# Optimization experiments

Measured on AMD Instinct MI355X. Metric: run time of the kernel, lower is better.

The kernel has to match this reference:

```python
import jax, jax.numpy as jnp
import numpy as np

N_NODES = 100000
N_EDGES = 1600000
IN_FEATS = 128
N_HIDDEN = 32
N_CLASSES = 47
HEADS = (4, 4)
NEG_SLOPE = 0.2


def setup_inputs() -> dict:
    key = jax.random.key(0)
    ks = jax.random.split(key, 12)
    x = jax.random.normal(ks[0], (N_NODES, IN_FEATS), dtype=jnp.float32)
    src = jax.random.randint(ks[1], (N_EDGES,), 0, N_NODES)
    dst = jax.random.randint(ks[2], (N_EDGES,), 0, N_NODES)
    inverse_idx = jax.random.randint(ks[3], (N_NODES,), 0, N_NODES)
    h1 = HEADS[0] * N_HIDDEN
    s1 = 1.0 / np.sqrt(IN_FEATS)
    W1 = jax.random.normal(ks[4], (IN_FEATS, h1), dtype=jnp.float32) * s1
    al1 = jax.random.normal(ks[5], (HEADS[0], N_HIDDEN), dtype=jnp.float32) * 0.1
    ar1 = jax.random.normal(ks[6], (HEADS[0], N_HIDDEN), dtype=jnp.float32) * 0.1
    b1 = jnp.zeros((h1,), dtype=jnp.float32)
    h2 = HEADS[1] * N_CLASSES
    s2 = 1.0 / np.sqrt(h1)
    W2 = jax.random.normal(ks[7], (h1, h2), dtype=jnp.float32) * s2
    al2 = jax.random.normal(ks[8], (HEADS[1], N_CLASSES), dtype=jnp.float32) * 0.1
    ar2 = jax.random.normal(ks[9], (HEADS[1], N_CLASSES), dtype=jnp.float32) * 0.1
    b2 = jnp.zeros((h2,), dtype=jnp.float32)
    return {"x": x, "src": src, "dst": dst, "inverse_idx": inverse_idx,
            "W1": W1, "al1": al1, "ar1": ar1, "b1": b1,
            "W2": W2, "al2": al2, "ar2": ar2, "b2": b2}


def gat_conv(h, src, dst, W, al, ar, b, heads, out_dim, apply_elu):
    # DGL GATConv (feat_drop=attn_drop=0, eval mode):
    # projected per-head features, edge attention, per-dst softmax, aggregate.
    feat = (h @ W).reshape(-1, heads, out_dim)               # (N, H, D)
    el = jnp.einsum('nhd,hd->nh', feat, al)                  # (N, H)
    er = jnp.einsum('nhd,hd->nh', feat, ar)                  # (N, H)
    e = el[src] + er[dst]                                    # (E, H)
    e = jnp.where(e > 0, e, NEG_SLOPE * e)                   # LeakyReLU
    m = jax.ops.segment_max(e, dst, num_segments=N_NODES)    # (N, H)
    m = jnp.where(jnp.isfinite(m), m, 0.0)
    ex = jnp.exp(e - m[dst])
    s = jax.ops.segment_sum(ex, dst, num_segments=N_NODES)   # (N, H)
    alpha = ex / jnp.maximum(s[dst], 1e-9)                   # (E, H)
    msg = feat[src] * alpha[:, :, None]                      # (E, H, D)
    out = jax.ops.segment_sum(msg, dst, num_segments=N_NODES)  # (N, H, D)
    out = out + b.reshape(1, heads, out_dim)
    if apply_elu:
        out = jax.nn.elu(out)
    return out


def reference(x, src, dst, inverse_idx, W1, al1, ar1, b1, W2, al2, ar2, b2):
    # Layer 0: GATConv + ELU, flatten heads, then NPFeatureShuffle reindex.
    h = gat_conv(x, src, dst, W1, al1, ar1, b1, HEADS[0], N_HIDDEN, True)
    h = h.reshape(N_NODES, HEADS[0] * N_HIDDEN)
    h = h[inverse_idx]  # cross-partition shuffle reindex
    # Layer 1: GATConv, no activation, mean over heads.
    h = gat_conv(h, src, dst, W2, al2, ar2, b2, HEADS[1], N_CLASSES, False)
    return h.mean(axis=1)  # (N, n_classes)
```

## Files before the change

kernel.cpp:

```cpp
#include <hip/hip_runtime.h>
#include <hip/hip_bf16.h>
#include <hip/hip_fp16.h>
#include <type_traits>

#define N_NODES 100000
#define N_EDGES 1600000
#define LOG2E 1.44269504f

typedef _Float16 half8_t __attribute__((ext_vector_type(8)));
typedef _Float16 half4_t __attribute__((ext_vector_type(4)));
typedef float floatx4 __attribute__((ext_vector_type(4)));

__global__ void csr_prep(const int* __restrict__ dst, int* __restrict__ deg, int E,
                         const float* __restrict__ W1, const float* __restrict__ W2,
                         const float* __restrict__ al1, const float* __restrict__ ar1,
                         const float* __restrict__ al2, const float* __restrict__ ar2,
                         __half* __restrict__ Wt1, __half* __restrict__ Wt2) {
    const int b = blockIdx.x;
    if (b < 6250) {
        int i = b * 256 + threadIdx.x;
        if (i < E) atomicAdd(&deg[dst[i]], 1);
        return;
    }
    const int c = b - 6250;
    const int k = threadIdx.x;
    if (k >= 128) return;
    if (c < 128) {
        Wt1[c * 128 + k] = __float2half(W1[k * 128 + c]);
    } else if (c < 144) {
        int j = c - 128;
        float v = 0.f;
        if (j < 8) {
            int h = j & 3;
            const float* a = (j < 4) ? al1 : ar1;
            for (int d = 0; d < 32; ++d)
                v = fmaf(W1[k * 128 + h * 32 + d], a[h * 32 + d], v);
        }
        Wt1[c * 128 + k] = __float2half(v * LOG2E);
    } else if (c < 336) {
        int c2 = c - 144;
        float v = (c2 < 188) ? W2[k * 188 + c2] : 0.f;
        Wt2[c2 * 128 + k] = __float2half(v);
    } else {
        int j = c - 336;
        float v = 0.f;
        if (j < 8) {
            int h = j & 3;
            const float* a = (j < 4) ? al2 : ar2;
            for (int d = 0; d < 47; ++d)
                v = fmaf(W2[k * 188 + h * 47 + d], a[h * 47 + d], v);
        }
        Wt2[(192 + j) * 128 + k] = __float2half(v * LOG2E);
    }
}

__global__ void block_sums(const int* __restrict__ deg, int* __restrict__ bsum, int N) {
    __shared__ int ws[4];
    const int t = threadIdx.x;
    int i = blockIdx.x * 256 + t;
    int v = (i < N) ? deg[i] : 0;
    #pragma unroll
    for (int o = 32; o; o >>= 1) v += __shfl_down(v, o, 64);
    if ((t & 63) == 0) ws[t >> 6] = v;
    __syncthreads();
    if (t == 0) bsum[blockIdx.x] = ws[0] + ws[1] + ws[2] + ws[3];
}

__global__ void scan_bsum(int* __restrict__ bsum, int nb) {
    __shared__ int sh[512];
    const int t = threadIdx.x;
    sh[t] = (t < nb) ? bsum[t] : 0;
    __syncthreads();
    for (int o = 1; o < 512; o <<= 1) {
        int v = (t >= o) ? sh[t - o] : 0;
        __syncthreads();
        sh[t] += v;
        __syncthreads();
    }
    if (t < nb) bsum[t] = sh[t];
}

__global__ void scan_final(const int* __restrict__ deg, const int* __restrict__ bsum,
                           int* __restrict__ row_ptr, int* __restrict__ cursor, int N) {
    __shared__ int ws[4];
    const int t = threadIdx.x;
    const int b = blockIdx.x;
    const int i = b * 256 + t;
    const int lane = t & 63;
    const int wid = t >> 6;
    int v = (i < N) ? deg[i] : 0;
    int x = v;
    #pragma unroll
    for (int o = 1; o < 64; o <<= 1) {
        int y = __shfl_up(x, o, 64);
        if (lane >= o) x += y;
    }
    if (lane == 63) ws[wid] = x;
    __syncthreads();
    int prefix = (b > 0) ? bsum[b - 1] : 0;
    for (int k = 0; k < wid; ++k) prefix += ws[k];
    if (i < N) {
        row_ptr[i + 1] = prefix + x;
        cursor[i] = prefix + x - v;
    }
    if (i == 0) row_ptr[0] = 0;
}

template <int TT, int NLOG, int OSTRIDE, bool EMBED, bool GATHER, typename AT>
__device__ __forceinline__ void gemm_body(
    int bx,
    const AT* __restrict__ A, const __half* __restrict__ Wt,
    __half* __restrict__ C, __half* __restrict__ elh, float* __restrict__ er,
    const int* __restrict__ gather, int N) {
    constexpr int LDA = 136;
    __shared__ _Float16 As[64 * LDA];
    __shared__ int ridx[64];
    const int tid = threadIdx.x;
    const int r0 = bx * 64;

    if (tid < 64) {
        int row = r0 + tid;
        int pr = 0;
        if (row < N) pr = GATHER ? gather[row] : row;
        ridx[tid] = pr;
    }
    __syncthreads();

    {
        const int r = tid >> 2, q = tid & 3;
        const int src = ridx[r];
        if constexpr (std::is_same<AT, float>::value) {
            const float4* A4 = (const float4*)A;
            #pragma unroll
            for (int i = 0; i < 8; ++i) {
                float4 v = A4[(size_t)src * 32 + q * 8 + i];
                half4_t hv = {(_Float16)v.x, (_Float16)v.y, (_Float16)v.z, (_Float16)v.w};
                *(half4_t*)&As[r * LDA + q * 32 + i * 4] = hv;
            }
        } else {
            const uint4* A4 = (const uint4*)A;
            #pragma unroll
            for (int i = 0; i < 4; ++i) {
                uint4 v = A4[(size_t)src * 16 + q * 4 + i];
                *(uint4*)&As[r * LDA + q * 32 + i * 8] = v;
            }
        }
    }
    __syncthreads();

    const int lane = tid & 63;
    const int wave = tid >> 6;
    const int col = lane & 15;
    const int quad = lane >> 4;
    const int arow = wave * 16 + col;

    floatx4 acc[TT];
    #pragma unroll
    for (int t = 0; t < TT; ++t) acc[t] = (floatx4){0.f, 0.f, 0.f, 0.f};

    #pragma unroll
    for (int kc = 0; kc < 4; ++kc) {
        half8_t a = *(const half8_t*)&As[arow * LDA + kc * 32 + quad * 8];
        #pragma unroll
        for (int t = 0; t < TT; ++t) {
            half8_t b = *(const half8_t*)&Wt[(size_t)(t * 16 + col) * 128 + kc * 32 + quad * 8];
            acc[t] = __builtin_amdgcn_mfma_f32_16x16x32_f16(a, b, acc[t], 0, 0, 0);
        }
    }

    #pragma unroll
    for (int t = 0; t < TT - 1; ++t) {
        #pragma unroll
        for (int r = 0; r < 4; ++r) {
            int row = r0 + wave * 16 + quad * 4 + r;
            int c = t * 16 + col;
            if (row < N && c < NLOG) {
                int sc = EMBED ? (c + c / 47) : c;
                C[(size_t)row * OSTRIDE + sc] = __float2half(acc[t][r]);
            }
        }
    }
    #pragma unroll
    for (int r = 0; r < 4; ++r) {
        int row = r0 + wave * 16 + quad * 4 + r;
        if (row < N) {
            if (col < 4) {
                elh[row * 4 + col] = __float2half(acc[TT - 1][r]);
                if constexpr (EMBED)
                    C[(size_t)row * OSTRIDE + col * 48 + 47] = __float2half(0.f);
            } else if (col < 8) {
                er[row * 4 + (col - 4)] = acc[TT - 1][r];
            }
        }
    }
}

template <int TT, int NLOG, int OSTRIDE, bool EMBED, bool GATHER, typename AT>
__global__ __launch_bounds__(256) void gemm_mfma(
    const AT* __restrict__ A, const __half* __restrict__ Wt,
    __half* __restrict__ C, __half* __restrict__ elh, float* __restrict__ er,
    const int* __restrict__ gather, int N) {
    gemm_body<TT, NLOG, OSTRIDE, EMBED, GATHER, AT>(blockIdx.x, A, Wt, C, elh, er, gather, N);
}

__global__ __launch_bounds__(256) void scatter_gemm1(
    const int* __restrict__ src, const int* __restrict__ dst,
    int* __restrict__ cursor, int* __restrict__ e_src, int E,
    const float* __restrict__ A, const __half* __restrict__ Wt,
    __half* __restrict__ C, __half* __restrict__ elh, float* __restrict__ er, int N) {
    const int g = blockIdx.x >> 3;
    if ((g & 1) == 0) {
        const int part = blockIdx.x & 7;
        const int sb = g >> 1;
        const int psz = N_NODES / 8;
        const int lo = part * psz;
        const int hi = lo + psz;
        const int SLICE = E / 200;
        const int4* d4 = (const int4*)(dst + sb * SLICE);
        const int4* s4 = (const int4*)(src + sb * SLICE);
        const int nvec = SLICE / 4;
        for (int v = threadIdx.x; v < nvec; v += 256) {
            int4 dd = d4[v];
            int4 ss = s4[v];
            if (dd.x >= lo && dd.x < hi) e_src[atomicAdd(&cursor[dd.x], 1)] = ss.x;
            if (dd.y >= lo && dd.y < hi) e_src[atomicAdd(&cursor[dd.y], 1)] = ss.y;
            if (dd.z >= lo && dd.z < hi) e_src[atomicAdd(&cursor[dd.z], 1)] = ss.z;
            if (dd.w >= lo && dd.w < hi) e_src[atomicAdd(&cursor[dd.w], 1)] = ss.w;
        }
    } else {
        const int bx = (g >> 1) * 8 + (blockIdx.x & 7);
        if (bx * 64 < N)
            gemm_body<9, 128, 128, false, false, float>(bx, A, Wt, C, elh, er, nullptr, N);
    }
}

__global__ __launch_bounds__(256) void gat_gather1(
    const __half* __restrict__ feat, const __half* __restrict__ elh,
    const float* __restrict__ er,
    const int* __restrict__ row_ptr, const int* __restrict__ e_src,
    const float* __restrict__ bias, __half* __restrict__ out) {
    const int t = threadIdx.x;
    const int lane = t & 63;
    const int n = blockIdx.x * 4 + (t >> 6);
    const int h = lane >> 4;
    const int start = row_ptr[n], end = row_ptr[n + 1];
    const char* fb = (const char*)feat;
    const uint32_t flo = (uint32_t)lane * 4u;
    const float ern = er[n * 4 + h];
    float ax = 0.f, ay = 0.f, s = 0.f;
    int i = start;
    for (; i + 4 <= end; i += 4) {
        int sv0 = e_src[i + 0], sv1 = e_src[i + 1], sv2 = e_src[i + 2], sv3 = e_src[i + 3];
        float e0 = __half2float(elh[sv0 * 4 + h]) + ern;
        float e1 = __half2float(elh[sv1 * 4 + h]) + ern;
        float e2 = __half2float(elh[sv2 * 4 + h]) + ern;
        float e3 = __half2float(elh[sv3 * 4 + h]) + ern;
        float w0 = exp2f(fmaxf(e0, 0.2f * e0));
        float w1 = exp2f(fmaxf(e1, 0.2f * e1));
        float w2 = exp2f(fmaxf(e2, 0.2f * e2));
        float w3 = exp2f(fmaxf(e3, 0.2f * e3));
        __half2 f0 = *(const __half2*)(fb + (uint32_t)sv0 * 256u + flo);
        __half2 f1 = *(const __half2*)(fb + (uint32_t)sv1 * 256u + flo);
        __half2 f2v = *(const __half2*)(fb + (uint32_t)sv2 * 256u + flo);
        __half2 f3 = *(const __half2*)(fb + (uint32_t)sv3 * 256u + flo);
        float2 g0 = __half22float2(f0), g1 = __half22float2(f1);
        float2 g2 = __half22float2(f2v), g3 = __half22float2(f3);
        s += (w0 + w1) + (w2 + w3);
        ax += w0 * g0.x + w1 * g1.x + w2 * g2.x + w3 * g3.x;
        ay += w0 * g0.y + w1 * g1.y + w2 * g2.y + w3 * g3.y;
    }
    for (; i < end; ++i) {
        int sv = e_src[i];
        float e = __half2float(elh[sv * 4 + h]) + ern;
        float ww = exp2f(fmaxf(e, 0.2f * e));
        float2 g = __half22float2(*(const __half2*)(fb + (uint32_t)sv * 256u + flo));
        s += ww;
        ax += ww * g.x;
        ay += ww * g.y;
    }
    float inv = 1.f / fmaxf(s, 1e-9f);
    float ox = ax * inv + bias[lane * 2 + 0];
    float oy = ay * inv + bias[lane * 2 + 1];
    ox = (ox > 0.f) ? ox : (__expf(ox) - 1.f);
    oy = (oy > 0.f) ? oy : (__expf(oy) - 1.f);
    ((__half2*)out)[(size_t)n * 64 + lane] = __floats2half2_rn(ox, oy);
}

__global__ __launch_bounds__(256) void gat_gather2(
    const __half* __restrict__ feat, const __half* __restrict__ elh,
    const float* __restrict__ er,
    const int* __restrict__ row_ptr, const int* __restrict__ e_src,
    const float* __restrict__ bias, float* __restrict__ out) {
    const int t = threadIdx.x;
    const int lane = t & 63;
    const int n = blockIdx.x * 4 + (t >> 6);
    if (lane < 48) {
        const int h = lane / 12;
        const int q = lane - h * 12;
        const int start = row_ptr[n], end = row_ptr[n + 1];
        const char* fb = (const char*)feat;
        const uint32_t flo = (uint32_t)lane * 8u;
        const float ern = er[n * 4 + h];
        float a0 = 0.f, a1 = 0.f, a2 = 0.f, a3 = 0.f, s = 0.f;
        int i = start;
        for (; i + 4 <= end; i += 4) {
            int sv0 = e_src[i + 0], sv1 = e_src[i + 1], sv2 = e_src[i + 2], sv3 = e_src[i + 3];
            float e0 = __half2float(elh[sv0 * 4 + h]) + ern;
            float e1 = __half2float(elh[sv1 * 4 + h]) + ern;
            float e2 = __half2float(elh[sv2 * 4 + h]) + ern;
            float e3 = __half2float(elh[sv3 * 4 + h]) + ern;
            float w0 = exp2f(fmaxf(e0, 0.2f * e0));
            float w1 = exp2f(fmaxf(e1, 0.2f * e1));
            float w2 = exp2f(fmaxf(e2, 0.2f * e2));
            float w3 = exp2f(fmaxf(e3, 0.2f * e3));
            half4_t f0 = *(const half4_t*)(fb + (uint32_t)sv0 * 384u + flo);
            half4_t f1 = *(const half4_t*)(fb + (uint32_t)sv1 * 384u + flo);
            half4_t f2 = *(const half4_t*)(fb + (uint32_t)sv2 * 384u + flo);
            half4_t f3 = *(const half4_t*)(fb + (uint32_t)sv3 * 384u + flo);
            s += (w0 + w1) + (w2 + w3);
            a0 += w0 * (float)f0[0] + w1 * (float)f1[0] + w2 * (float)f2[0] + w3 * (float)f3[0];
            a1 += w0 * (float)f0[1] + w1 * (float)f1[1] + w2 * (float)f2[1] + w3 * (float)f3[1];
            a2 += w0 * (float)f0[2] + w1 * (float)f1[2] + w2 * (float)f2[2] + w3 * (float)f3[2];
            a3 += w0 * (float)f0[3] + w1 * (float)f1[3] + w2 * (float)f2[3] + w3 * (float)f3[3];
        }
        for (; i < end; ++i) {
            int sv = e_src[i];
            float e = __half2float(elh[sv * 4 + h]) + ern;
            float ww = exp2f(fmaxf(e, 0.2f * e));
            half4_t f0 = *(const half4_t*)(fb + (uint32_t)sv * 384u + flo);
            s += ww;
            a0 += ww * (float)f0[0];
            a1 += ww * (float)f0[1];
            a2 += ww * (float)f0[2];
            a3 += ww * (float)f0[3];
        }
        float inv = 1.f / fmaxf(s, 1e-9f);
        const int d0 = q * 4;
        float b0 = bias[h * 47 + d0 + 0];
        float b1 = bias[h * 47 + d0 + 1];
        float b2 = bias[h * 47 + d0 + 2];
        float b3 = (d0 + 3 < 47) ? bias[h * 47 + d0 + 3] : 0.f;
        float r0 = a0 * inv + b0;
        float r1 = a1 * inv + b1;
        float r2 = a2 * inv + b2;
        float r3 = a3 * inv + b3;
        float t0 = r0 + __shfl(r0, lane + 12, 64) + __shfl(r0, lane + 24, 64) + __shfl(r0, lane + 36, 64);
        float t1 = r1 + __shfl(r1, lane + 12, 64) + __shfl(r1, lane + 24, 64) + __shfl(r1, lane + 36, 64);
        float t2 = r2 + __shfl(r2, lane + 12, 64) + __shfl(r2, lane + 24, 64) + __shfl(r2, lane + 36, 64);
        float t3 = r3 + __shfl(r3, lane + 12, 64) + __shfl(r3, lane + 24, 64) + __shfl(r3, lane + 36, 64);
        if (h == 0) {
            size_t base = (size_t)n * 47 + d0;
            out[base + 0] = 0.25f * t0;
            out[base + 1] = 0.25f * t1;
            out[base + 2] = 0.25f * t2;
            if (d0 + 3 < 47) out[base + 3] = 0.25f * t3;
        }
    }
}

extern "C" void kernel_launch(void* const* d_in, const int* in_sizes, int n_in,
                              void* d_out, int out_size, void* d_ws, size_t ws_size,
                              hipStream_t stream) {
    const int N = N_NODES, E = N_EDGES;
    const float* x    = (const float*)d_in[0];
    const int*   src  = (const int*)d_in[1];
    const int*   dst  = (const int*)d_in[2];
    const int*   inv  = (const int*)d_in[3];
    const float* W1   = (const float*)d_in[4];
    const float* al1  = (const float*)d_in[5];
    const float* ar1  = (const float*)d_in[6];
    const float* b1   = (const float*)d_in[7];
    const float* W2   = (const float*)d_in[8];
    const float* al2  = (const float*)d_in[9];
    const float* ar2  = (const float*)d_in[10];
    const float* b2   = (const float*)d_in[11];
    float* out = (float*)d_out;

    char* p = (char*)d_ws;
    auto carve = [&](size_t bytes) {
        char* q = p;
        p += (bytes + 255) & ~size_t(255);
        return q;
    };
    __half* feat1   = (__half*)carve((size_t)N * 128 * 2);
    __half* feat2   = (__half*)carve((size_t)N * 192 * 2);
    __half* hbuf    = (__half*)carve((size_t)N * 128 * 2);
    __half* Wt1     = (__half*)carve(144 * 128 * 2);
    __half* Wt2     = (__half*)carve(208 * 128 * 2);
    __half* elh1    = (__half*)carve((size_t)N * 4 * 2);
    __half* elh2    = (__half*)carve((size_t)N * 4 * 2);
    float*  er      = (float*)carve((size_t)N * 4 * 4);
    int*    deg     = (int*)carve((size_t)N * 4);
    int*    row_ptr = (int*)carve((size_t)(N + 1) * 4);
    int*    cursor  = (int*)carve((size_t)N * 4);
    int*    bsum    = (int*)carve(512 * 4);
    int*    e_src   = (int*)carve((size_t)E * 4);

    const int nb = (N + 255) / 256;

    hipMemsetAsync(deg, 0, (size_t)N * 4, stream);
    csr_prep<<<6250 + 352, 256, 0, stream>>>(dst, deg, E, W1, W2, al1, ar1, al2, ar2, Wt1, Wt2);
    block_sums<<<nb, 256, 0, stream>>>(deg, bsum, N);
    scan_bsum<<<1, 512, 0, stream>>>(bsum, nb);
    scan_final<<<nb, 256, 0, stream>>>(deg, bsum, row_ptr, cursor, N);

    scatter_gemm1<<<3200, 256, 0, stream>>>(src, dst, cursor, e_src, E,
                                            x, Wt1, feat1, elh1, er, N);

    gat_gather1<<<(N + 3) / 4, 256, 0, stream>>>(feat1, elh1, er, row_ptr, e_src, b1, hbuf);

    gemm_mfma<13, 188, 192, true, true, __half><<<(N + 63) / 64, 256, 0, stream>>>(
        hbuf, Wt2, feat2, elh2, er, inv, N);
    gat_gather2<<<(N + 3) / 4, 256, 0, stream>>>(feat2, elh2, er, row_ptr, e_src, b2, out);
}
```

Measured before the change: 508.2 us.

## Embed layer-2 source logits in feature padding and co-schedule GEMM1 with degree count

Stores the layer-2 el attention logit in each head's unused padding slot (column 47) of feat2. The gather then reads it from the feature vector it already loads and broadcasts it with a shuffle, removing a separate random elh2 load per edge. It also moves the layer-1 GEMM out of the scatter kernel into a new kernel that interleaves it with degree counting, and makes the edge scatter a standalone kernel. The cost is extra shuffles in the gather loop, plus a new kernel schedule that may balance or overlap the work differently.

```diff
diff --git a/kernel.cpp b/kernel.cpp
--- a/kernel.cpp
+++ b/kernel.cpp
@@ -11,20 +11,12 @@
 typedef _Float16 half4_t __attribute__((ext_vector_type(4)));
 typedef float floatx4 __attribute__((ext_vector_type(4)));
 
-__global__ void csr_prep(const int* __restrict__ dst, int* __restrict__ deg, int E,
-                         const float* __restrict__ W1, const float* __restrict__ W2,
-                         const float* __restrict__ al1, const float* __restrict__ ar1,
-                         const float* __restrict__ al2, const float* __restrict__ ar2,
-                         __half* __restrict__ Wt1, __half* __restrict__ Wt2) {
-    const int b = blockIdx.x;
-    if (b < 6250) {
-        int i = b * 256 + threadIdx.x;
-        if (i < E) atomicAdd(&deg[dst[i]], 1);
-        return;
-    }
-    const int c = b - 6250;
+__global__ void prep_w(const float* __restrict__ W1, const float* __restrict__ W2,
+                       const float* __restrict__ al1, const float* __restrict__ ar1,
+                       const float* __restrict__ al2, const float* __restrict__ ar2,
+                       __half* __restrict__ Wt1, __half* __restrict__ Wt2) {
+    const int c = blockIdx.x;
     const int k = threadIdx.x;
-    if (k >= 128) return;
     if (c < 128) {
         Wt1[c * 128 + k] = __float2half(W1[k * 128 + c]);
     } else if (c < 144) {
@@ -185,9 +177,10 @@
         int row = r0 + wave * 16 + quad * 4 + r;
         if (row < N) {
             if (col < 4) {
-                elh[row * 4 + col] = __float2half(acc[TT - 1][r]);
                 if constexpr (EMBED)
-                    C[(size_t)row * OSTRIDE + col * 48 + 47] = __float2half(0.f);
+                    C[(size_t)row * OSTRIDE + col * 48 + 47] = __float2half(acc[TT - 1][r]);
+                else
+                    elh[row * 4 + col] = __float2half(acc[TT - 1][r]);
             } else if (col < 8) {
                 er[row * 4 + (col - 4)] = acc[TT - 1][r];
             }
@@ -203,34 +196,41 @@
     gemm_body<TT, NLOG, OSTRIDE, EMBED, GATHER, AT>(blockIdx.x, A, Wt, C, elh, er, gather, N);
 }
 
-__global__ __launch_bounds__(256) void scatter_gemm1(
-    const int* __restrict__ src, const int* __restrict__ dst,
-    int* __restrict__ cursor, int* __restrict__ e_src, int E,
+__global__ __launch_bounds__(256) void count_gemm1(
+    const int* __restrict__ dst, int* __restrict__ deg, int E,
     const float* __restrict__ A, const __half* __restrict__ Wt,
     __half* __restrict__ C, __half* __restrict__ elh, float* __restrict__ er, int N) {
-    const int g = blockIdx.x >> 3;
-    if ((g & 1) == 0) {
-        const int part = blockIdx.x & 7;
-        const int sb = g >> 1;
-        const int psz = N_NODES / 8;
-        const int lo = part * psz;
-        const int hi = lo + psz;
-        const int SLICE = E / 200;
-        const int4* d4 = (const int4*)(dst + sb * SLICE);
-        const int4* s4 = (const int4*)(src + sb * SLICE);
-        const int nvec = SLICE / 4;
-        for (int v = threadIdx.x; v < nvec; v += 256) {
-            int4 dd = d4[v];
-            int4 ss = s4[v];
-            if (dd.x >= lo && dd.x < hi) e_src[atomicAdd(&cursor[dd.x], 1)] = ss.x;
-            if (dd.y >= lo && dd.y < hi) e_src[atomicAdd(&cursor[dd.y], 1)] = ss.y;
-            if (dd.z >= lo && dd.z < hi) e_src[atomicAdd(&cursor[dd.z], 1)] = ss.z;
-            if (dd.w >= lo && dd.w < hi) e_src[atomicAdd(&cursor[dd.w], 1)] = ss.w;
-        }
-    } else {
-        const int bx = (g >> 1) * 8 + (blockIdx.x & 7);
+    const int bid = blockIdx.x;
+    if (bid % 5 == 0) {
+        const int bx = bid / 5;
         if (bx * 64 < N)
             gemm_body<9, 128, 128, false, false, float>(bx, A, Wt, C, elh, er, nullptr, N);
+    } else {
+        const int cid = bid - bid / 5 - 1;
+        int i = cid * 256 + threadIdx.x;
+        if (i < E) atomicAdd(&deg[dst[i]], 1);
+    }
+}
+
+__global__ __launch_bounds__(256) void scatter_edges_part(
+    const int* __restrict__ src, const int* __restrict__ dst,
+    int* __restrict__ cursor, int* __restrict__ e_src, int E) {
+    const int part = blockIdx.x & 7;
+    const int sb = blockIdx.x >> 3;
+    const int psz = N_NODES / 8;
+    const int lo = part * psz;
+    const int hi = lo + psz;
+    const int SLICE = E / 200;
+    const int4* d4 = (const int4*)(dst + sb * SLICE);
+    const int4* s4 = (const int4*)(src + sb * SLICE);
+    const int nvec = SLICE / 4;
+    for (int v = threadIdx.x; v < nvec; v += 256) {
+        int4 dd = d4[v];
+        int4 ss = s4[v];
+        if (dd.x >= lo && dd.x < hi) e_src[atomicAdd(&cursor[dd.x], 1)] = ss.x;
+        if (dd.y >= lo && dd.y < hi) e_src[atomicAdd(&cursor[dd.y], 1)] = ss.y;
+        if (dd.z >= lo && dd.z < hi) e_src[atomicAdd(&cursor[dd.z], 1)] = ss.z;
+        if (dd.w >= lo && dd.w < hi) e_src[atomicAdd(&cursor[dd.w], 1)] = ss.w;
     }
 }
 
@@ -287,8 +287,7 @@
 }
 
 __global__ __launch_bounds__(256) void gat_gather2(
-    const __half* __restrict__ feat, const __half* __restrict__ elh,
-    const float* __restrict__ er,
+    const __half* __restrict__ feat, const float* __restrict__ er,
     const int* __restrict__ row_ptr, const int* __restrict__ e_src,
     const float* __restrict__ bias, float* __restrict__ out) {
     const int t = threadIdx.x;
@@ -297,6 +296,7 @@
     if (lane < 48) {
         const int h = lane / 12;
         const int q = lane - h * 12;
+        const int g11 = h * 12 + 11;
         const int start = row_ptr[n], end = row_ptr[n + 1];
         const char* fb = (const char*)feat;
         const uint32_t flo = (uint32_t)lane * 8u;
@@ -305,18 +305,18 @@
         int i = start;
         for (; i + 4 <= end; i += 4) {
             int sv0 = e_src[i + 0], sv1 = e_src[i + 1], sv2 = e_src[i + 2], sv3 = e_src[i + 3];
-            float e0 = __half2float(elh[sv0 * 4 + h]) + ern;
-            float e1 = __half2float(elh[sv1 * 4 + h]) + ern;
-            float e2 = __half2float(elh[sv2 * 4 + h]) + ern;
-            float e3 = __half2float(elh[sv3 * 4 + h]) + ern;
+            half4_t f0 = *(const half4_t*)(fb + (uint32_t)sv0 * 384u + flo);
+            half4_t f1 = *(const half4_t*)(fb + (uint32_t)sv1 * 384u + flo);
+            half4_t f2 = *(const half4_t*)(fb + (uint32_t)sv2 * 384u + flo);
+            half4_t f3 = *(const half4_t*)(fb + (uint32_t)sv3 * 384u + flo);
+            float e0 = __shfl((float)f0[3], g11, 64) + ern;
+            float e1 = __shfl((float)f1[3], g11, 64) + ern;
+            float e2 = __shfl((float)f2[3], g11, 64) + ern;
+            float e3 = __shfl((float)f3[3], g11, 64) + ern;
             float w0 = exp2f(fmaxf(e0, 0.2f * e0));
             float w1 = exp2f(fmaxf(e1, 0.2f * e1));
             float w2 = exp2f(fmaxf(e2, 0.2f * e2));
             float w3 = exp2f(fmaxf(e3, 0.2f * e3));
-            half4_t f0 = *(const half4_t*)(fb + (uint32_t)sv0 * 384u + flo);
-            half4_t f1 = *(const half4_t*)(fb + (uint32_t)sv1 * 384u + flo);
-            half4_t f2 = *(const half4_t*)(fb + (uint32_t)sv2 * 384u + flo);
-            half4_t f3 = *(const half4_t*)(fb + (uint32_t)sv3 * 384u + flo);
             s += (w0 + w1) + (w2 + w3);
             a0 += w0 * (float)f0[0] + w1 * (float)f1[0] + w2 * (float)f2[0] + w3 * (float)f3[0];
             a1 += w0 * (float)f0[1] + w1 * (float)f1[1] + w2 * (float)f2[1] + w3 * (float)f3[1];
@@ -325,15 +325,16 @@
         }
         for (; i < end; ++i) {
             int sv = e_src[i];
-            float e = __half2float(elh[sv * 4 + h]) + ern;
+            half4_t f0 = *(const half4_t*)(fb + (uint32_t)sv * 384u + flo);
+            float e = __shfl((float)f0[3], g11, 64) + ern;
             float ww = exp2f(fmaxf(e, 0.2f * e));
-            half4_t f0 = *(const half4_t*)(fb + (uint32_t)sv * 384u + flo);
             s += ww;
             a0 += ww * (float)f0[0];
             a1 += ww * (float)f0[1];
             a2 += ww * (float)f0[2];
             a3 += ww * (float)f0[3];
         }
+        if (q == 11) a3 = 0.f;
         float inv = 1.f / fmaxf(s, 1e-9f);
         const int d0 = q * 4;
         float b0 = bias[h * 47 + d0 + 0];
@@ -388,7 +389,6 @@
     __half* Wt1     = (__half*)carve(144 * 128 * 2);
     __half* Wt2     = (__half*)carve(208 * 128 * 2);
     __half* elh1    = (__half*)carve((size_t)N * 4 * 2);
-    __half* elh2    = (__half*)carve((size_t)N * 4 * 2);
     float*  er      = (float*)carve((size_t)N * 4 * 4);
     int*    deg     = (int*)carve((size_t)N * 4);
     int*    row_ptr = (int*)carve((size_t)(N + 1) * 4);
@@ -399,17 +399,19 @@
     const int nb = (N + 255) / 256;
 
     hipMemsetAsync(deg, 0, (size_t)N * 4, stream);
-    csr_prep<<<6250 + 352, 256, 0, stream>>>(dst, deg, E, W1, W2, al1, ar1, al2, ar2, Wt1, Wt2);
+    prep_w<<<352, 128, 0, stream>>>(W1, W2, al1, ar1, al2, ar2, Wt1, Wt2);
+
+    count_gemm1<<<7813, 256, 0, stream>>>(dst, deg, E, x, Wt1, feat1, elh1, er, N);
+
     block_sums<<<nb, 256, 0, stream>>>(deg, bsum, N);
     scan_bsum<<<1, 512, 0, stream>>>(bsum, nb);
     scan_final<<<nb, 256, 0, stream>>>(deg, bsum, row_ptr, cursor, N);
 
-    scatter_gemm1<<<3200, 256, 0, stream>>>(src, dst, cursor, e_src, E,
-                                            x, Wt1, feat1, elh1, er, N);
+    scatter_edges_part<<<1600, 256, 0, stream>>>(src, dst, cursor, e_src, E);
 
     gat_gather1<<<(N + 3) / 4, 256, 0, stream>>>(feat1, elh1, er, row_ptr, e_src, b1, hbuf);
 
     gemm_mfma<13, 188, 192, true, true, __half><<<(N + 63) / 64, 256, 0, stream>>>(
-        hbuf, Wt2, feat2, elh2, er, inv, N);
-    gat_gather2<<<(N + 3) / 4, 256, 0, stream>>>(feat2, elh2, er, row_ptr, e_src, b2, out);
-}
+        hbuf, Wt2, feat2, nullptr, er, inv, N);
+    gat_gather2<<<(N + 3) / 4, 256, 0, stream>>>(feat2, er, row_ptr, e_src, b2, out);
+}
```

After: 507.8 us. About the same (-0.1%).

## Precompute normalized edge attention weights in a separate kernel before gathers

Applied to the files above, without the earlier changes.

Adds a wk_alpha kernel that computes each edge's softmax weight per head, already normalized, into a 4xE float buffer. Both gather kernels then read these weights as aligned float4 loads instead of recomputing exp and the running sum in the inner loop. The aim is to remove the elh gathers and exp work from the latency-bound gather loops. The cost is two extra kernel launches, a 25.6MB write and read of weights, and a second pass over e_src and elh.

```diff
diff --git a/kernel.cpp b/kernel.cpp
--- a/kernel.cpp
+++ b/kernel.cpp
@@ -234,9 +234,35 @@
     }
 }
 
+__global__ __launch_bounds__(256) void wk_alpha(
+    const __half* __restrict__ elh, const float* __restrict__ er,
+    const int* __restrict__ row_ptr, const int* __restrict__ e_src,
+    float* __restrict__ wbuf) {
+    const int n = blockIdx.x * 4 + (threadIdx.x >> 6);
+    const int lane = threadIdx.x & 63;
+    const int h = lane >> 4;
+    const int e = lane & 15;
+    const int start = row_ptr[n], end = row_ptr[n + 1];
+    const float ern = er[n * 4 + h];
+    float s = 0.f;
+    for (int i = start + e; i < end; i += 16) {
+        int sv = e_src[i];
+        float x = __half2float(elh[sv * 4 + h]) + ern;
+        s += exp2f(fmaxf(x, 0.2f * x));
+    }
+    #pragma unroll
+    for (int o = 1; o < 16; o <<= 1) s += __shfl_xor(s, o, 64);
+    const float inv = 1.f / fmaxf(s, 1e-9f);
+    float* wp = wbuf + h * N_EDGES;
+    for (int i = start + e; i < end; i += 16) {
+        int sv = e_src[i];
+        float x = __half2float(elh[sv * 4 + h]) + ern;
+        wp[i] = exp2f(fmaxf(x, 0.2f * x)) * inv;
+    }
+}
+
 __global__ __launch_bounds__(256) void gat_gather1(
-    const __half* __restrict__ feat, const __half* __restrict__ elh,
-    const float* __restrict__ er,
+    const __half* __restrict__ feat, const float* __restrict__ wbuf,
     const int* __restrict__ row_ptr, const int* __restrict__ e_src,
     const float* __restrict__ bias, __half* __restrict__ out) {
     const int t = threadIdx.x;
@@ -246,49 +272,46 @@
     const int start = row_ptr[n], end = row_ptr[n + 1];
     const char* fb = (const char*)feat;
     const uint32_t flo = (uint32_t)lane * 4u;
-    const float ern = er[n * 4 + h];
-    float ax = 0.f, ay = 0.f, s = 0.f;
+    const float* wp = wbuf + h * N_EDGES;
+    float ax = 0.f, ay = 0.f;
     int i = start;
+    int pre = (4 - (start & 3)) & 3;
+    if (pre > end - start) pre = end - start;
+    for (int k = 0; k < pre; ++k, ++i) {
+        int sv = e_src[i];
+        float ww = wp[i];
+        float2 g = __half22float2(*(const __half2*)(fb + (uint32_t)sv * 256u + flo));
+        ax += ww * g.x;
+        ay += ww * g.y;
+    }
     for (; i + 4 <= end; i += 4) {
+        float4 w = *(const float4*)(wp + i);
         int sv0 = e_src[i + 0], sv1 = e_src[i + 1], sv2 = e_src[i + 2], sv3 = e_src[i + 3];
-        float e0 = __half2float(elh[sv0 * 4 + h]) + ern;
-        float e1 = __half2float(elh[sv1 * 4 + h]) + ern;
-        float e2 = __half2float(elh[sv2 * 4 + h]) + ern;
-        float e3 = __half2float(elh[sv3 * 4 + h]) + ern;
-        float w0 = exp2f(fmaxf(e0, 0.2f * e0));
-        float w1 = exp2f(fmaxf(e1, 0.2f * e1));
-        float w2 = exp2f(fmaxf(e2, 0.2f * e2));
-        float w3 = exp2f(fmaxf(e3, 0.2f * e3));
         __half2 f0 = *(const __half2*)(fb + (uint32_t)sv0 * 256u + flo);
         __half2 f1 = *(const __half2*)(fb + (uint32_t)sv1 * 256u + flo);
         __half2 f2v = *(const __half2*)(fb + (uint32_t)sv2 * 256u + flo);
         __half2 f3 = *(const __half2*)(fb + (uint32_t)sv3 * 256u + flo);
         float2 g0 = __half22float2(f0), g1 = __half22float2(f1);
         float2 g2 = __half22float2(f2v), g3 = __half22float2(f3);
-        s += (w0 + w1) + (w2 + w3);
-        ax += w0 * g0.x + w1 * g1.x + w2 * g2.x + w3 * g3.x;
-        ay += w0 * g0.y + w1 * g1.y + w2 * g2.y + w3 * g3.y;
+        ax += w.x * g0.x + w.y * g1.x + w.z * g2.x + w.w * g3.x;
+        ay += w.x * g0.y + w.y * g1.y + w.z * g2.y + w.w * g3.y;
     }
     for (; i < end; ++i) {
         int sv = e_src[i];
-        float e = __half2float(elh[sv * 4 + h]) + ern;
-        float ww = exp2f(fmaxf(e, 0.2f * e));
+        float ww = wp[i];
         float2 g = __half22float2(*(const __half2*)(fb + (uint32_t)sv * 256u + flo));
-        s += ww;
         ax += ww * g.x;
         ay += ww * g.y;
     }
-    float inv = 1.f / fmaxf(s, 1e-9f);
-    float ox = ax * inv + bias[lane * 2 + 0];
-    float oy = ay * inv + bias[lane * 2 + 1];
+    float ox = ax + bias[lane * 2 + 0];
+    float oy = ay + bias[lane * 2 + 1];
     ox = (ox > 0.f) ? ox : (__expf(ox) - 1.f);
     oy = (oy > 0.f) ? oy : (__expf(oy) - 1.f);
     ((__half2*)out)[(size_t)n * 64 + lane] = __floats2half2_rn(ox, oy);
 }
 
 __global__ __launch_bounds__(256) void gat_gather2(
-    const __half* __restrict__ feat, const __half* __restrict__ elh,
-    const float* __restrict__ er,
+    const __half* __restrict__ feat, const float* __restrict__ wbuf,
     const int* __restrict__ row_ptr, const int* __restrict__ e_src,
     const float* __restrict__ bias, float* __restrict__ out) {
     const int t = threadIdx.x;
@@ -300,50 +323,51 @@
         const int start = row_ptr[n], end = row_ptr[n + 1];
         const char* fb = (const char*)feat;
         const uint32_t flo = (uint32_t)lane * 8u;
-        const float ern = er[n * 4 + h];
-        float a0 = 0.f, a1 = 0.f, a2 = 0.f, a3 = 0.f, s = 0.f;
+        const float* wp = wbuf + h * N_EDGES;
+        float a0 = 0.f, a1 = 0.f, a2 = 0.f, a3 = 0.f;
         int i = start;
+        int pre = (4 - (start & 3)) & 3;
+        if (pre > end - start) pre = end - start;
+        for (int k = 0; k < pre; ++k, ++i) {
+            int sv = e_src[i];
+            float ww = wp[i];
+            half4_t f0 = *(const half4_t*)(fb + (uint32_t)sv * 384u + flo);
+            a0 += ww * (float)f0[0];
+            a1 += ww * (float)f0[1];
+            a2 += ww * (float)f0[2];
+            a3 += ww * (float)f0[3];
+        }
         for (; i + 4 <= end; i += 4) {
+            float4 w = *(const float4*)(wp + i);
             int sv0 = e_src[i + 0], sv1 = e_src[i + 1], sv2 = e_src[i + 2], sv3 = e_src[i + 3];
-            float e0 = __half2float(elh[sv0 * 4 + h]) + ern;
-            float e1 = __half2float(elh[sv1 * 4 + h]) + ern;
-            float e2 = __half2float(elh[sv2 * 4 + h]) + ern;
-            float e3 = __half2float(elh[sv3 * 4 + h]) + ern;
-            float w0 = exp2f(fmaxf(e0, 0.2f * e0));
-            float w1 = exp2f(fmaxf(e1, 0.2f * e1));
-            float w2 = exp2f(fmaxf(e2, 0.2f * e2));
-            float w3 = exp2f(fmaxf(e3, 0.2f * e3));
             half4_t f0 = *(const half4_t*)(fb + (uint32_t)sv0 * 384u + flo);
             half4_t f1 = *(const half4_t*)(fb + (uint32_t)sv1 * 384u + flo);
             half4_t f2 = *(const half4_t*)(fb + (uint32_t)sv2 * 384u + flo);
             half4_t f3 = *(const half4_t*)(fb + (uint32_t)sv3 * 384u + flo);
-            s += (w0 + w1) + (w2 + w3);
-            a0 += w0 * (float)f0[0] + w1 * (float)f1[0] + w2 * (float)f2[0] + w3 * (float)f3[0];
-            a1 += w0 * (float)f0[1] + w1 * (float)f1[1] + w2 * (float)f2[1] + w3 * (float)f3[1];
-            a2 += w0 * (float)f0[2] + w1 * (float)f1[2] + w2 * (float)f2[2] + w3 * (float)f3[2];
-            a3 += w0 * (float)f0[3] + w1 * (float)f1[3] + w2 * (float)f2[3] + w3 * (float)f3[3];
+            a0 += w.x * (float)f0[0] + w.y * (float)f1[0] + w.z * (float)f2[0] + w.w * (float)f3[0];
+            a1 += w.x * (float)f0[1] + w.y * (float)f1[1] + w.z * (float)f2[1] + w.w * (float)f3[1];
+            a2 += w.x * (float)f0[2] + w.y * (float)f1[2] + w.z * (float)f2[2] + w.w * (float)f3[2];
+            a3 += w.x * (float)f0[3] + w.y * (float)f1[3] + w.z * (float)f2[3] + w.w * (float)f3[3];
         }
         for (; i < end; ++i) {
             int sv = e_src[i];
-            float e = __half2float(elh[sv * 4 + h]) + ern;
-            float ww = exp2f(fmaxf(e, 0.2f * e));
+            float ww = wp[i];
             half4_t f0 = *(const half4_t*)(fb + (uint32_t)sv * 384u + flo);
-            s += ww;
             a0 += ww * (float)f0[0];
             a1 += ww * (float)f0[1];
             a2 += ww * (float)f0[2];
             a3 += ww * (float)f0[3];
         }
-        float inv = 1.f / fmaxf(s, 1e-9f);
+        if (q == 11) a3 = 0.f;
         const int d0 = q * 4;
         float b0 = bias[h * 47 + d0 + 0];
         float b1 = bias[h * 47 + d0 + 1];
         float b2 = bias[h * 47 + d0 + 2];
         float b3 = (d0 + 3 < 47) ? bias[h * 47 + d0 + 3] : 0.f;
-        float r0 = a0 * inv + b0;
-        float r1 = a1 * inv + b1;
-        float r2 = a2 * inv + b2;
-        float r3 = a3 * inv + b3;
+        float r0 = a0 + b0;
+        float r1 = a1 + b1;
+        float r2 = a2 + b2;
+        float r3 = a3 + b3;
         float t0 = r0 + __shfl(r0, lane + 12, 64) + __shfl(r0, lane + 24, 64) + __shfl(r0, lane + 36, 64);
         float t1 = r1 + __shfl(r1, lane + 12, 64) + __shfl(r1, lane + 24, 64) + __shfl(r1, lane + 36, 64);
         float t2 = r2 + __shfl(r2, lane + 12, 64) + __shfl(r2, lane + 24, 64) + __shfl(r2, lane + 36, 64);
@@ -395,6 +419,7 @@
     int*    cursor  = (int*)carve((size_t)N * 4);
     int*    bsum    = (int*)carve(512 * 4);
     int*    e_src   = (int*)carve((size_t)E * 4);
+    float*  wbuf    = (float*)carve((size_t)4 * E * 4);
 
     const int nb = (N + 255) / 256;
 
@@ -407,9 +432,11 @@
     scatter_gemm1<<<3200, 256, 0, stream>>>(src, dst, cursor, e_src, E,
                                             x, Wt1, feat1, elh1, er, N);
 
-    gat_gather1<<<(N + 3) / 4, 256, 0, stream>>>(feat1, elh1, er, row_ptr, e_src, b1, hbuf);
+    wk_alpha<<<N / 4, 256, 0, stream>>>(elh1, er, row_ptr, e_src, wbuf);
+    gat_gather1<<<(N + 3) / 4, 256, 0, stream>>>(feat1, wbuf, row_ptr, e_src, b1, hbuf);
 
     gemm_mfma<13, 188, 192, true, true, __half><<<(N + 63) / 64, 256, 0, stream>>>(
         hbuf, Wt2, feat2, elh2, er, inv, N);
-    gat_gather2<<<(N + 3) / 4, 256, 0, stream>>>(feat2, elh2, er, row_ptr, e_src, b2, out);
-}
+    wk_alpha<<<N / 4, 256, 0, stream>>>(elh2, er, row_ptr, e_src, wbuf);
+    gat_gather2<<<(N + 3) / 4, 256, 0, stream>>>(feat2, wbuf, row_ptr, e_src, b2, out);
+}
```

New measurement: 591.1 us. 16.3% more time.

## Embed layer-2 attention logits in feature padding slot and use nontemporal loads

Applied to the files above, without the earlier changes.

The second-layer GEMM now writes each head's source attention logit into the unused 48th padding slot of the feature row instead of a separate elh2 array. The layer-2 gather reads it from the feature vector it already loads and broadcasts it across the head's lanes with a shuffle, then zeroes that lane's accumulator. This removes one dependent random gather per edge. Streaming loads of edge arrays, e_src and GEMM inputs are also marked nontemporal to reduce cache pollution, which could instead hurt if that data would have been reused.

```diff
diff --git a/kernel.cpp b/kernel.cpp
--- a/kernel.cpp
+++ b/kernel.cpp
@@ -10,6 +10,8 @@
 typedef _Float16 half8_t __attribute__((ext_vector_type(8)));
 typedef _Float16 half4_t __attribute__((ext_vector_type(4)));
 typedef float floatx4 __attribute__((ext_vector_type(4)));
+typedef int intx4 __attribute__((ext_vector_type(4)));
+typedef unsigned int uintx4 __attribute__((ext_vector_type(4)));
 
 __global__ void csr_prep(const int* __restrict__ dst, int* __restrict__ deg, int E,
                          const float* __restrict__ W1, const float* __restrict__ W2,
@@ -19,7 +21,7 @@
     const int b = blockIdx.x;
     if (b < 6250) {
         int i = b * 256 + threadIdx.x;
-        if (i < E) atomicAdd(&deg[dst[i]], 1);
+        if (i < E) atomicAdd(&deg[__builtin_nontemporal_load(dst + i)], 1);
         return;
     }
     const int c = b - 6250;
@@ -130,19 +132,19 @@
         const int r = tid >> 2, q = tid & 3;
         const int src = ridx[r];
         if constexpr (std::is_same<AT, float>::value) {
-            const float4* A4 = (const float4*)A;
+            const floatx4* A4 = (const floatx4*)A;
             #pragma unroll
             for (int i = 0; i < 8; ++i) {
-                float4 v = A4[(size_t)src * 32 + q * 8 + i];
+                floatx4 v = __builtin_nontemporal_load(&A4[(size_t)src * 32 + q * 8 + i]);
                 half4_t hv = {(_Float16)v.x, (_Float16)v.y, (_Float16)v.z, (_Float16)v.w};
                 *(half4_t*)&As[r * LDA + q * 32 + i * 4] = hv;
             }
         } else {
-            const uint4* A4 = (const uint4*)A;
+            const uintx4* A4 = (const uintx4*)A;
             #pragma unroll
             for (int i = 0; i < 4; ++i) {
-                uint4 v = A4[(size_t)src * 16 + q * 4 + i];
-                *(uint4*)&As[r * LDA + q * 32 + i * 8] = v;
+                uintx4 v = __builtin_nontemporal_load(&A4[(size_t)src * 16 + q * 4 + i]);
+                *(uintx4*)&As[r * LDA + q * 32 + i * 8] = v;
             }
         }
     }
@@ -185,9 +187,10 @@
         int row = r0 + wave * 16 + quad * 4 + r;
         if (row < N) {
             if (col < 4) {
-                elh[row * 4 + col] = __float2half(acc[TT - 1][r]);
                 if constexpr (EMBED)
-                    C[(size_t)row * OSTRIDE + col * 48 + 47] = __float2half(0.f);
+                    C[(size_t)row * OSTRIDE + col * 48 + 47] = __float2half(acc[TT - 1][r]);
+                else
+                    elh[row * 4 + col] = __float2half(acc[TT - 1][r]);
             } else if (col < 8) {
                 er[row * 4 + (col - 4)] = acc[TT - 1][r];
             }
@@ -216,12 +219,12 @@
         const int lo = part * psz;
         const int hi = lo + psz;
         const int SLICE = E / 200;
-        const int4* d4 = (const int4*)(dst + sb * SLICE);
-        const int4* s4 = (const int4*)(src + sb * SLICE);
+        const intx4* d4 = (const intx4*)(dst + sb * SLICE);
+        const intx4* s4 = (const intx4*)(src + sb * SLICE);
         const int nvec = SLICE / 4;
         for (int v = threadIdx.x; v < nvec; v += 256) {
-            int4 dd = d4[v];
-            int4 ss = s4[v];
+            intx4 dd = __builtin_nontemporal_load(&d4[v]);
+            intx4 ss = __builtin_nontemporal_load(&s4[v]);
             if (dd.x >= lo && dd.x < hi) e_src[atomicAdd(&cursor[dd.x], 1)] = ss.x;
             if (dd.y >= lo && dd.y < hi) e_src[atomicAdd(&cursor[dd.y], 1)] = ss.y;
             if (dd.z >= lo && dd.z < hi) e_src[atomicAdd(&cursor[dd.z], 1)] = ss.z;
@@ -250,7 +253,10 @@
     float ax = 0.f, ay = 0.f, s = 0.f;
     int i = start;
     for (; i + 4 <= end; i += 4) {
-        int sv0 = e_src[i + 0], sv1 = e_src[i + 1], sv2 = e_src[i + 2], sv3 = e_src[i + 3];
+        int sv0 = __builtin_nontemporal_load(e_src + i + 0);
+        int sv1 = __builtin_nontemporal_load(e_src + i + 1);
+        int sv2 = __builtin_nontemporal_load(e_src + i + 2);
+        int sv3 = __builtin_nontemporal_load(e_src + i + 3);
         float e0 = __half2float(elh[sv0 * 4 + h]) + ern;
         float e1 = __half2float(elh[sv1 * 4 + h]) + ern;
         float e2 = __half2float(elh[sv2 * 4 + h]) + ern;
@@ -287,8 +293,7 @@
 }
 
 __global__ __launch_bounds__(256) void gat_gather2(
-    const __half* __restrict__ feat, const __half* __restrict__ elh,
-    const float* __restrict__ er,
+    const __half* __restrict__ feat, const float* __restrict__ er,
     const int* __restrict__ row_ptr, const int* __restrict__ e_src,
     const float* __restrict__ bias, float* __restrict__ out) {
     const int t = threadIdx.x;
@@ -297,6 +302,7 @@
     if (lane < 48) {
         const int h = lane / 12;
         const int q = lane - h * 12;
+        const int g11 = h * 12 + 11;
         const int start = row_ptr[n], end = row_ptr[n + 1];
         const char* fb = (const char*)feat;
         const uint32_t flo = (uint32_t)lane * 8u;
@@ -304,19 +310,22 @@
         float a0 = 0.f, a1 = 0.f, a2 = 0.f, a3 = 0.f, s = 0.f;
         int i = start;
         for (; i + 4 <= end; i += 4) {
-            int sv0 = e_src[i + 0], sv1 = e_src[i + 1], sv2 = e_src[i + 2], sv3 = e_src[i + 3];
-            float e0 = __half2float(elh[sv0 * 4 + h]) + ern;
-            float e1 = __half2float(elh[sv1 * 4 + h]) + ern;
-            float e2 = __half2float(elh[sv2 * 4 + h]) + ern;
-            float e3 = __half2float(elh[sv3 * 4 + h]) + ern;
+            int sv0 = __builtin_nontemporal_load(e_src + i + 0);
+            int sv1 = __builtin_nontemporal_load(e_src + i + 1);
+            int sv2 = __builtin_nontemporal_load(e_src + i + 2);
+            int sv3 = __builtin_nontemporal_load(e_src + i + 3);
+            half4_t f0 = *(const half4_t*)(fb + (uint32_t)sv0 * 384u + flo);
+            half4_t f1 = *(const half4_t*)(fb + (uint32_t)sv1 * 384u + flo);
+            half4_t f2 = *(const half4_t*)(fb + (uint32_t)sv2 * 384u + flo);
+            half4_t f3 = *(const half4_t*)(fb + (uint32_t)sv3 * 384u + flo);
+            float e0 = __shfl((float)f0[3], g11, 64) + ern;
+            float e1 = __shfl((float)f1[3], g11, 64) + ern;
+            float e2 = __shfl((float)f2[3], g11, 64) + ern;
+            float e3 = __shfl((float)f3[3], g11, 64) + ern;
             float w0 = exp2f(fmaxf(e0, 0.2f * e0));
             float w1 = exp2f(fmaxf(e1, 0.2f * e1));
             float w2 = exp2f(fmaxf(e2, 0.2f * e2));
             float w3 = exp2f(fmaxf(e3, 0.2f * e3));
-            half4_t f0 = *(const half4_t*)(fb + (uint32_t)sv0 * 384u + flo);
-            half4_t f1 = *(const half4_t*)(fb + (uint32_t)sv1 * 384u + flo);
-            half4_t f2 = *(const half4_t*)(fb + (uint32_t)sv2 * 384u + flo);
-            half4_t f3 = *(const half4_t*)(fb + (uint32_t)sv3 * 384u + flo);
             s += (w0 + w1) + (w2 + w3);
             a0 += w0 * (float)f0[0] + w1 * (float)f1[0] + w2 * (float)f2[0] + w3 * (float)f3[0];
             a1 += w0 * (float)f0[1] + w1 * (float)f1[1] + w2 * (float)f2[1] + w3 * (float)f3[1];
@@ -325,15 +334,16 @@
         }
         for (; i < end; ++i) {
             int sv = e_src[i];
-            float e = __half2float(elh[sv * 4 + h]) + ern;
+            half4_t f0 = *(const half4_t*)(fb + (uint32_t)sv * 384u + flo);
+            float e = __shfl((float)f0[3], g11, 64) + ern;
             float ww = exp2f(fmaxf(e, 0.2f * e));
-            half4_t f0 = *(const half4_t*)(fb + (uint32_t)sv * 384u + flo);
             s += ww;
             a0 += ww * (float)f0[0];
             a1 += ww * (float)f0[1];
             a2 += ww * (float)f0[2];
             a3 += ww * (float)f0[3];
         }
+        if (q == 11) a3 = 0.f;
         float inv = 1.f / fmaxf(s, 1e-9f);
         const int d0 = q * 4;
         float b0 = bias[h * 47 + d0 + 0];
@@ -388,7 +398,6 @@
     __half* Wt1     = (__half*)carve(144 * 128 * 2);
     __half* Wt2     = (__half*)carve(208 * 128 * 2);
     __half* elh1    = (__half*)carve((size_t)N * 4 * 2);
-    __half* elh2    = (__half*)carve((size_t)N * 4 * 2);
     float*  er      = (float*)carve((size_t)N * 4 * 4);
     int*    deg     = (int*)carve((size_t)N * 4);
     int*    row_ptr = (int*)carve((size_t)(N + 1) * 4);
@@ -410,6 +419,6 @@
     gat_gather1<<<(N + 3) / 4, 256, 0, stream>>>(feat1, elh1, er, row_ptr, e_src, b1, hbuf);
 
     gemm_mfma<13, 188, 192, true, true, __half><<<(N + 63) / 64, 256, 0, stream>>>(
-        hbuf, Wt2, feat2, elh2, er, inv, N);
-    gat_gather2<<<(N + 3) / 4, 256, 0, stream>>>(feat2, elh2, er, row_ptr, e_src, b2, out);
-}
+        hbuf, Wt2, feat2, nullptr, er, inv, N);
+    gat_gather2<<<(N + 3) / 4, 256, 0, stream>>>(feat2, er, row_ptr, e_src, b2, out);
+}
```

Result: slower. 564.2 us (+11.0%).
